# Optimization experiments

Measured on AMD Instinct MI355X. Metric: run time of the kernel, lower is better.

## Reference

```python
import jax, jax.numpy as jnp
import numpy as np

N_NODES = 100000
N_EDGES = 3200000
EMB_DIM = 128


def setup_inputs() -> dict:
    key = jax.random.key(0)
    k_emb, k_w1, k_w2, k_e = jax.random.split(key, 4)
    emb = jax.random.normal(k_emb, (N_NODES, EMB_DIM), dtype=jnp.float32)
    W1 = jax.random.normal(k_w1, (EMB_DIM, 64), dtype=jnp.float32) * (1.0 / np.sqrt(EMB_DIM))
    b1 = jnp.zeros((64,), dtype=jnp.float32)
    W2 = jax.random.normal(k_w2, (64, 32), dtype=jnp.float32) * (1.0 / np.sqrt(64))
    b2 = jnp.zeros((32,), dtype=jnp.float32)
    edge_index = jax.random.randint(k_e, (2, N_EDGES), 0, N_NODES, dtype=jnp.int64)
    return {"embedding": emb, "W1": W1, "b1": b1, "W2": W2, "b2": b2,
            "edge_index": edge_index}


def gcn_conv(x, W, b, src, dst, n):
    # PyG GCNConv defaults: add self-loops, symmetric normalization D^-1/2 (A+I) D^-1/2,
    # linear transform first, then gather-scale-scatter aggregation, then bias.
    xw = x @ W                                                  # [N, out]
    ones = jnp.ones(src.shape, dtype=xw.dtype)
    deg = jax.ops.segment_sum(ones, dst, num_segments=n) + 1.0  # in-degree + self-loop
    dis = jax.lax.rsqrt(deg)                                    # deg >= 1 always
    norm = dis[src] * dis[dst]                                  # [E]
    agg = jax.ops.segment_sum(xw[src] * norm[:, None], dst, num_segments=n)
    agg = agg + (dis * dis)[:, None] * xw                       # self-loop messages
    return agg + b


def reference(embedding, W1, b1, W2, b2, edge_index):
    n = embedding.shape[0]
    src, dst = edge_index[0], edge_index[1]
    # encode
    h = jax.nn.relu(gcn_conv(embedding, W1, b1, src, dst, n))
    z = gcn_conv(h, W2, b2, src, dst, n)                        # [N, 32]
    # decode: per-edge gather-dot-sigmoid
    logits = jnp.sum(z[src] * z[dst], axis=1)                   # [E]
    return jax.nn.sigmoid(logits)
```

## Files before the change

kernel.cpp:

```cpp
#include <hip/hip_runtime.h>
#include <hip/hip_bf16.h>
#include <math.h>

#define NN 100000
#define NE 3200000
#define NPAD 100096
#define NB 196
#define BN 512
#define EPB 8192
#define NBLK 391

__device__ __forceinline__ unsigned short bf16_of(float x) {
    __hip_bfloat16 h = __float2bfloat16(x);
    return *(unsigned short*)&h;
}
__device__ __forceinline__ unsigned pack2(float a, float b) {
    return (unsigned)bf16_of(a) | ((unsigned)bf16_of(b) << 16);
}
__device__ __forceinline__ float lo_f(unsigned u) { return __uint_as_float(u << 16); }
__device__ __forceinline__ float hi_f(unsigned u) { return __uint_as_float(u & 0xffff0000u); }
__device__ __forceinline__ void acc8(float* a, uint4 r) {
    a[0] += lo_f(r.x); a[1] += hi_f(r.x);
    a[2] += lo_f(r.y); a[3] += hi_f(r.y);
    a[4] += lo_f(r.z); a[5] += hi_f(r.z);
    a[6] += lo_f(r.w); a[7] += hi_f(r.w);
}

__global__ __launch_bounds__(256) void hist_kernel(const int* __restrict__ dst,
                                                   int* __restrict__ blkhist) {
    __shared__ int cnt[NB];
    int t = threadIdx.x;
    for (int i = t; i < NB; i += 256) cnt[i] = 0;
    __syncthreads();
    int e0 = blockIdx.x * EPB;
    int e1 = min(e0 + EPB, NE);
    for (int e = e0 + t; e < e1; e += 256) atomicAdd(&cnt[dst[e] >> 9], 1);
    __syncthreads();
    for (int i = t; i < NB; i += 256) blkhist[i * NBLK + blockIdx.x] = cnt[i];
}

__global__ __launch_bounds__(64) void scanA_kernel(int* __restrict__ blkhist,
                                                   int* __restrict__ totals) {
    int j = blockIdx.x, lane = threadIdx.x;
    int base = j * NBLK;
    int carry = 0;
    for (int c = 0; c < NBLK; c += 64) {
        int b = c + lane;
        int v = (b < NBLK) ? blkhist[base + b] : 0;
        int inc = v;
#pragma unroll
        for (int m = 1; m < 64; m <<= 1) {
            int u = __shfl_up(inc, m, 64);
            if (lane >= m) inc += u;
        }
        if (b < NBLK) blkhist[base + b] = carry + inc - v;
        carry += __shfl(inc, 63, 64);
    }
    if (lane == 0) totals[j] = carry;
}

__global__ __launch_bounds__(256) void scanB_kernel(const int* __restrict__ totals,
                                                    int* __restrict__ bucket_base) {
    __shared__ int sm[NB];
    int t = threadIdx.x;
    if (t < NB) sm[t] = totals[t];
    __syncthreads();
    if (t == 0) {
        int r = 0;
        for (int i = 0; i < NB; ++i) { bucket_base[i] = r; r += sm[i]; }
        bucket_base[NB] = r;
    }
}

__global__ __launch_bounds__(256) void scatter_kernel(const int* __restrict__ src,
                                                      const int* __restrict__ dst,
                                                      const int* __restrict__ blkhist,
                                                      const int* __restrict__ bucket_base,
                                                      int* __restrict__ staged) {
    __shared__ int cur[NB];
    int t = threadIdx.x;
    for (int i = t; i < NB; i += 256)
        cur[i] = bucket_base[i] + blkhist[i * NBLK + blockIdx.x];
    __syncthreads();
    int e0 = blockIdx.x * EPB;
    int e1 = min(e0 + EPB, NE);
    for (int e = e0 + t; e < e1; e += 256) {
        int s = src[e], d = dst[e];
        int p = atomicAdd(&cur[d >> 9], 1);
        staged[p] = (s << 9) | (d & (BN - 1));
    }
}

__global__ __launch_bounds__(256) void fine_kernel(const int* __restrict__ staged,
                                                   const int* __restrict__ bucket_base,
                                                   int* __restrict__ offset,
                                                   float* __restrict__ dis,
                                                   int* __restrict__ csr_src) {
    __shared__ int hist[BN];
    __shared__ int offs[BN];
    __shared__ int cur[BN];
    int t = threadIdx.x, j = blockIdx.x;
    int bb = bucket_base[j], be = bucket_base[j + 1];
    for (int i = t; i < BN; i += 256) hist[i] = 0;
    __syncthreads();
    for (int e = bb + t; e < be; e += 256) atomicAdd(&hist[staged[e] & (BN - 1)], 1);
    __syncthreads();
    if (t < 64) {
        int v[8]; int s = 0;
#pragma unroll
        for (int k = 0; k < 8; ++k) { v[k] = hist[t * 8 + k]; s += v[k]; }
        int inc = s;
#pragma unroll
        for (int m = 1; m < 64; m <<= 1) {
            int u = __shfl_up(inc, m, 64);
            if (t >= m) inc += u;
        }
        int run = inc - s;
#pragma unroll
        for (int k = 0; k < 8; ++k) { offs[t * 8 + k] = run; run += v[k]; }
    }
    __syncthreads();
    for (int l = t; l < BN; l += 256) {
        cur[l] = offs[l];
        int n = j * BN + l;
        if (n < NN) {
            offset[n] = bb + offs[l];
            dis[n] = rsqrtf((float)hist[l] + 1.0f);
        }
    }
    if (j == NB - 1 && t == 0) offset[NN] = NE;
    __syncthreads();
    for (int e = bb + t; e < be; e += 256) {
        int p = staged[e];
        int r = atomicAdd(&cur[p & (BN - 1)], 1);
        csr_src[bb + r] = p >> 9;
    }
}

__global__ __launch_bounds__(256) void mm1_kernel(const float* __restrict__ x,
                                                  const float* __restrict__ W,
                                                  const float* __restrict__ dis,
                                                  unsigned short* __restrict__ y) {
    __shared__ float Ws[128 * 64];
    __shared__ float xs[4][4][132];
    int t = threadIdx.x;
    for (int i = t; i < 128 * 64; i += 256) Ws[i] = W[i];
    int wave = t >> 6, lane = t & 63;
    int nsub = lane >> 4;
    int o4 = (lane & 15) * 4;
    int base = blockIdx.x * 16 + wave * 4;
#pragma unroll
    for (int r = 0; r < 4; ++r) {
        xs[wave][r][lane] = x[(size_t)(base + r) * 128 + lane];
        xs[wave][r][lane + 64] = x[(size_t)(base + r) * 128 + 64 + lane];
    }
    __syncthreads();
    float4 acc = {0.f, 0.f, 0.f, 0.f};
#pragma unroll 16
    for (int k = 0; k < 128; ++k) {
        float a = xs[wave][nsub][k];
        const float4 w = *(const float4*)&Ws[k * 64 + o4];
        acc.x = fmaf(a, w.x, acc.x);
        acc.y = fmaf(a, w.y, acc.y);
        acc.z = fmaf(a, w.z, acc.z);
        acc.w = fmaf(a, w.w, acc.w);
    }
    float sc = dis[base + nsub];
    ushort4 o;
    o.x = bf16_of(acc.x * sc); o.y = bf16_of(acc.y * sc);
    o.z = bf16_of(acc.z * sc); o.w = bf16_of(acc.w * sc);
    *(ushort4*)&y[(size_t)(base + nsub) * 64 + o4] = o;
}

__global__ __launch_bounds__(256) void mm2_kernel(const float* __restrict__ h,
                                                  const float* __restrict__ W,
                                                  const float* __restrict__ dis,
                                                  unsigned short* __restrict__ y) {
    __shared__ float Ws[64 * 32];
    __shared__ float hs[4][8][68];
    int t = threadIdx.x;
    for (int i = t; i < 64 * 32; i += 256) Ws[i] = W[i];
    int wave = t >> 6, lane = t & 63;
    int nsub = lane >> 3;
    int o4 = (lane & 7) * 4;
    int base = blockIdx.x * 32 + wave * 8;
#pragma unroll
    for (int r = 0; r < 8; ++r)
        hs[wave][r][lane] = h[(size_t)(base + r) * 64 + lane];
    __syncthreads();
    float4 acc = {0.f, 0.f, 0.f, 0.f};
#pragma unroll 16
    for (int k = 0; k < 64; ++k) {
        float a = hs[wave][nsub][k];
        const float4 w = *(const float4*)&Ws[k * 32 + o4];
        acc.x = fmaf(a, w.x, acc.x);
        acc.y = fmaf(a, w.y, acc.y);
        acc.z = fmaf(a, w.z, acc.z);
        acc.w = fmaf(a, w.w, acc.w);
    }
    float sc = dis[base + nsub];
    ushort4 o;
    o.x = bf16_of(acc.x * sc); o.y = bf16_of(acc.y * sc);
    o.z = bf16_of(acc.z * sc); o.w = bf16_of(acc.w * sc);
    *(ushort4*)&y[(size_t)(base + nsub) * 32 + o4] = o;
}

__global__ __launch_bounds__(256) void agg64_kernel(const uint4* __restrict__ ys4,
                                                    const float* __restrict__ dis,
                                                    const int* __restrict__ offset,
                                                    const int* __restrict__ csr_src,
                                                    const float* __restrict__ b,
                                                    float* __restrict__ h) {
    int tid = blockIdx.x * 256 + threadIdx.x;
    int nd = tid >> 3, c = tid & 7;
    if (nd >= NN) return;
    int start = offset[nd], end = offset[nd + 1];
    float acc[8] = {0, 0, 0, 0, 0, 0, 0, 0};
    acc8(acc, ys4[(size_t)nd * 8 + c]);
    int i = start;
    int n4 = start + ((end - start) & ~3);
    for (; i < n4; i += 4) {
        int s0 = csr_src[i], s1 = csr_src[i + 1], s2 = csr_src[i + 2], s3 = csr_src[i + 3];
        uint4 r0 = ys4[(size_t)s0 * 8 + c];
        uint4 r1 = ys4[(size_t)s1 * 8 + c];
        uint4 r2 = ys4[(size_t)s2 * 8 + c];
        uint4 r3 = ys4[(size_t)s3 * 8 + c];
        acc8(acc, r0); acc8(acc, r1); acc8(acc, r2); acc8(acc, r3);
    }
    for (; i < end; ++i) acc8(acc, ys4[(size_t)csr_src[i] * 8 + c]);
    float ds = dis[nd];
    const float4 bv0 = *(const float4*)&b[c * 8];
    const float4 bv1 = *(const float4*)&b[c * 8 + 4];
    float4 o0, o1;
    o0.x = fmaxf(fmaf(ds, acc[0], bv0.x), 0.f);
    o0.y = fmaxf(fmaf(ds, acc[1], bv0.y), 0.f);
    o0.z = fmaxf(fmaf(ds, acc[2], bv0.z), 0.f);
    o0.w = fmaxf(fmaf(ds, acc[3], bv0.w), 0.f);
    o1.x = fmaxf(fmaf(ds, acc[4], bv1.x), 0.f);
    o1.y = fmaxf(fmaf(ds, acc[5], bv1.y), 0.f);
    o1.z = fmaxf(fmaf(ds, acc[6], bv1.z), 0.f);
    o1.w = fmaxf(fmaf(ds, acc[7], bv1.w), 0.f);
    float* hp = &h[(size_t)nd * 64 + c * 8];
    *(float4*)hp = o0;
    *(float4*)(hp + 4) = o1;
}

__global__ __launch_bounds__(256) void agg32_kernel(const uint4* __restrict__ ys4,
                                                    const float* __restrict__ dis,
                                                    const int* __restrict__ offset,
                                                    const int* __restrict__ csr_src,
                                                    const float* __restrict__ b,
                                                    uint4* __restrict__ z4) {
    int tid = blockIdx.x * 256 + threadIdx.x;
    int nd = tid >> 2, c = tid & 3;
    if (nd >= NN) return;
    int start = offset[nd], end = offset[nd + 1];
    float acc[8] = {0, 0, 0, 0, 0, 0, 0, 0};
    acc8(acc, ys4[(size_t)nd * 4 + c]);
    int i = start;
    int n4 = start + ((end - start) & ~3);
    for (; i < n4; i += 4) {
        int s0 = csr_src[i], s1 = csr_src[i + 1], s2 = csr_src[i + 2], s3 = csr_src[i + 3];
        uint4 r0 = ys4[(size_t)s0 * 4 + c];
        uint4 r1 = ys4[(size_t)s1 * 4 + c];
        uint4 r2 = ys4[(size_t)s2 * 4 + c];
        uint4 r3 = ys4[(size_t)s3 * 4 + c];
        acc8(acc, r0); acc8(acc, r1); acc8(acc, r2); acc8(acc, r3);
    }
    for (; i < end; ++i) acc8(acc, ys4[(size_t)csr_src[i] * 4 + c]);
    float ds = dis[nd];
    const float4 bv0 = *(const float4*)&b[c * 8];
    const float4 bv1 = *(const float4*)&b[c * 8 + 4];
    uint4 o;
    o.x = pack2(fmaf(ds, acc[0], bv0.x), fmaf(ds, acc[1], bv0.y));
    o.y = pack2(fmaf(ds, acc[2], bv0.z), fmaf(ds, acc[3], bv0.w));
    o.z = pack2(fmaf(ds, acc[4], bv1.x), fmaf(ds, acc[5], bv1.y));
    o.w = pack2(fmaf(ds, acc[6], bv1.z), fmaf(ds, acc[7], bv1.w));
    z4[(size_t)nd * 4 + c] = o;
}

__global__ __launch_bounds__(256) void decode_kernel(const uint4* __restrict__ z4,
                                                     const int* __restrict__ src,
                                                     const int* __restrict__ dst,
                                                     float* __restrict__ out) {
    int tid = blockIdx.x * 256 + threadIdx.x;
    int e = tid >> 2, k = tid & 3;
    if (e >= NE) return;
    int s = src[e], d = dst[e];
    uint4 ra = z4[(size_t)s * 4 + k];
    uint4 rb = z4[(size_t)d * 4 + k];
    float acc;
    acc  = lo_f(ra.x) * lo_f(rb.x) + hi_f(ra.x) * hi_f(rb.x);
    acc += lo_f(ra.y) * lo_f(rb.y) + hi_f(ra.y) * hi_f(rb.y);
    acc += lo_f(ra.z) * lo_f(rb.z) + hi_f(ra.z) * hi_f(rb.z);
    acc += lo_f(ra.w) * lo_f(rb.w) + hi_f(ra.w) * hi_f(rb.w);
#pragma unroll
    for (int m = 2; m >= 1; m >>= 1) acc += __shfl_xor(acc, m, 4);
    if (k == 0) out[e] = 1.0f / (1.0f + expf(-acc));
}

extern "C" void kernel_launch(void* const* d_in, const int* in_sizes, int n_in,
                              void* d_out, int out_size, void* d_ws, size_t ws_size,
                              hipStream_t stream) {
    const float* emb = (const float*)d_in[0];
    const float* W1  = (const float*)d_in[1];
    const float* b1  = (const float*)d_in[2];
    const float* W2  = (const float*)d_in[3];
    const float* b2  = (const float*)d_in[4];
    const int*   ei  = (const int*)d_in[5];
    const int* src = ei;
    const int* dst = ei + NE;
    float* out = (float*)d_out;

    char* w = (char*)d_ws;
    int*   offset      = (int*)w;           w += (size_t)NPAD * 4;
    float* dis         = (float*)w;         w += (size_t)NPAD * 4;
    int*   bucket_base = (int*)w;           w += 1024;
    int*   totals      = (int*)w;           w += 1024;
    int*   blkhist     = (int*)w;           w += 307200;
    int*   csr_src     = (int*)w;           w += (size_t)NE * 4;
    int*   staged      = (int*)w;           w += (size_t)NE * 4;
    unsigned short* ysbuf = (unsigned short*)w; w += (size_t)NN * 64 * 2;
    float* h           = (float*)w;
    unsigned short* ys1 = ysbuf;
    unsigned short* ys2 = ysbuf;
    unsigned short* z   = ysbuf + (size_t)NN * 32;

    hist_kernel<<<NBLK, 256, 0, stream>>>(dst, blkhist);
    scanA_kernel<<<NB, 64, 0, stream>>>(blkhist, totals);
    scanB_kernel<<<1, 256, 0, stream>>>(totals, bucket_base);
    scatter_kernel<<<NBLK, 256, 0, stream>>>(src, dst, blkhist, bucket_base, staged);
    fine_kernel<<<NB, 256, 0, stream>>>(staged, bucket_base, offset, dis, csr_src);

    mm1_kernel<<<NN / 16, 256, 0, stream>>>(emb, W1, dis, ys1);
    agg64_kernel<<<(NN * 8) / 256, 256, 0, stream>>>((const uint4*)ys1, dis, offset, csr_src, b1, h);

    mm2_kernel<<<NN / 32, 256, 0, stream>>>(h, W2, dis, ys2);
    agg32_kernel<<<(NN * 4 + 255) / 256, 256, 0, stream>>>((const uint4*)ys2, dis, offset, csr_src, b2, (uint4*)z);

    decode_kernel<<<(NE * 4) / 256, 256, 0, stream>>>((const uint4*)z, src, dst, out);
}
```

Before: 401.0 us.

## Stage scatter in LDS, store hidden layer as bf16, widen matmul and gather unroll

```diff
diff --git a/kernel.cpp b/kernel.cpp
--- a/kernel.cpp
+++ b/kernel.cpp
@@ -77,17 +77,49 @@
                                                       const int* __restrict__ blkhist,
                                                       const int* __restrict__ bucket_base,
                                                       int* __restrict__ staged) {
-    __shared__ int cur[NB];
-    int t = threadIdx.x;
-    for (int i = t; i < NB; i += 256)
-        cur[i] = bucket_base[i] + blkhist[i * NBLK + blockIdx.x];
+    __shared__ int cnt[NB];
+    __shared__ int lbase[NB + 1];
+    __shared__ int gbase[NB];
+    __shared__ int sbuf[EPB];
+    int t = threadIdx.x;
+    for (int i = t; i < NB; i += 256) cnt[i] = 0;
     __syncthreads();
     int e0 = blockIdx.x * EPB;
     int e1 = min(e0 + EPB, NE);
+    int cn = e1 - e0;
+    for (int e = e0 + t; e < e1; e += 256) atomicAdd(&cnt[dst[e] >> 9], 1);
+    __syncthreads();
+    if (t < 64) {
+        int v[4]; int s = 0;
+#pragma unroll
+        for (int k = 0; k < 4; ++k) { int idx = t * 4 + k; v[k] = (idx < NB) ? cnt[idx] : 0; s += v[k]; }
+        int inc = s;
+#pragma unroll
+        for (int m = 1; m < 64; m <<= 1) {
+            int u = __shfl_up(inc, m, 64);
+            if (t >= m) inc += u;
+        }
+        int run = inc - s;
+#pragma unroll
+        for (int k = 0; k < 4; ++k) { int idx = t * 4 + k; if (idx < NB) lbase[idx] = run; run += v[k]; }
+        if (t == 63) lbase[NB] = inc;
+    }
+    __syncthreads();
+    for (int i = t; i < NB; i += 256) {
+        gbase[i] = bucket_base[i] + blkhist[i * NBLK + blockIdx.x];
+        cnt[i] = lbase[i];
+    }
+    __syncthreads();
     for (int e = e0 + t; e < e1; e += 256) {
         int s = src[e], d = dst[e];
-        int p = atomicAdd(&cur[d >> 9], 1);
-        staged[p] = (s << 9) | (d & (BN - 1));
+        int r = atomicAdd(&cnt[d >> 9], 1);
+        sbuf[r] = (s << 9) | (d & (BN - 1));
+    }
+    __syncthreads();
+    for (int i = t; i < cn; i += 256) {
+        int lo = 0, hi = NB - 1;
+        while (lo < hi) { int mid = (lo + hi + 1) >> 1; if (lbase[mid] <= i) lo = mid; else hi = mid - 1; }
+        staged[gbase[lo] + i - lbase[lo]] = sbuf[i];
     }
 }
 
@@ -142,37 +174,40 @@
                                                   const float* __restrict__ dis,
                                                   unsigned short* __restrict__ y) {
     __shared__ float Ws[128 * 64];
-    __shared__ float xs[4][4][132];
+    __shared__ float xs[4][8][132];
     int t = threadIdx.x;
     for (int i = t; i < 128 * 64; i += 256) Ws[i] = W[i];
     int wave = t >> 6, lane = t & 63;
-    int nsub = lane >> 4;
-    int o4 = (lane & 15) * 4;
-    int base = blockIdx.x * 16 + wave * 4;
-#pragma unroll
-    for (int r = 0; r < 4; ++r) {
+    int nsub = lane >> 3;
+    int o8 = (lane & 7) * 8;
+    int base = blockIdx.x * 32 + wave * 8;
+#pragma unroll
+    for (int r = 0; r < 8; ++r) {
         xs[wave][r][lane] = x[(size_t)(base + r) * 128 + lane];
         xs[wave][r][lane + 64] = x[(size_t)(base + r) * 128 + 64 + lane];
     }
     __syncthreads();
-    float4 acc = {0.f, 0.f, 0.f, 0.f};
+    float acc[8] = {0, 0, 0, 0, 0, 0, 0, 0};
 #pragma unroll 16
     for (int k = 0; k < 128; ++k) {
         float a = xs[wave][nsub][k];
-        const float4 w = *(const float4*)&Ws[k * 64 + o4];
-        acc.x = fmaf(a, w.x, acc.x);
-        acc.y = fmaf(a, w.y, acc.y);
-        acc.z = fmaf(a, w.z, acc.z);
-        acc.w = fmaf(a, w.w, acc.w);
+        const float4 w0 = *(const float4*)&Ws[k * 64 + o8];
+        const float4 w1 = *(const float4*)&Ws[k * 64 + o8 + 4];
+        acc[0] = fmaf(a, w0.x, acc[0]); acc[1] = fmaf(a, w0.y, acc[1]);
+        acc[2] = fmaf(a, w0.z, acc[2]); acc[3] = fmaf(a, w0.w, acc[3]);
+        acc[4] = fmaf(a, w1.x, acc[4]); acc[5] = fmaf(a, w1.y, acc[5]);
+        acc[6] = fmaf(a, w1.z, acc[6]); acc[7] = fmaf(a, w1.w, acc[7]);
     }
     float sc = dis[base + nsub];
-    ushort4 o;
-    o.x = bf16_of(acc.x * sc); o.y = bf16_of(acc.y * sc);
-    o.z = bf16_of(acc.z * sc); o.w = bf16_of(acc.w * sc);
-    *(ushort4*)&y[(size_t)(base + nsub) * 64 + o4] = o;
-}
-
-__global__ __launch_bounds__(256) void mm2_kernel(const float* __restrict__ h,
+    uint4 o;
+    o.x = pack2(acc[0] * sc, acc[1] * sc);
+    o.y = pack2(acc[2] * sc, acc[3] * sc);
+    o.z = pack2(acc[4] * sc, acc[5] * sc);
+    o.w = pack2(acc[6] * sc, acc[7] * sc);
+    *(uint4*)&y[(size_t)(base + nsub) * 64 + o8] = o;
+}
+
+__global__ __launch_bounds__(256) void mm2_kernel(const unsigned short* __restrict__ h,
                                                   const float* __restrict__ W,
                                                   const float* __restrict__ dis,
                                                   unsigned short* __restrict__ y) {
@@ -184,9 +219,14 @@
     int nsub = lane >> 3;
     int o4 = (lane & 7) * 4;
     int base = blockIdx.x * 32 + wave * 8;
-#pragma unroll
-    for (int r = 0; r < 8; ++r)
-        hs[wave][r][lane] = h[(size_t)(base + r) * 64 + lane];
+    const unsigned* h2 = (const unsigned*)h;
+#pragma unroll
+    for (int rr = 0; rr < 4; ++rr) {
+        int r = rr * 2 + (lane >> 5);
+        unsigned u = h2[(size_t)(base + r) * 32 + (lane & 31)];
+        hs[wave][r][(lane & 31) * 2] = lo_f(u);
+        hs[wave][r][(lane & 31) * 2 + 1] = hi_f(u);
+    }
     __syncthreads();
     float4 acc = {0.f, 0.f, 0.f, 0.f};
 #pragma unroll 16
@@ -210,7 +250,7 @@
                                                     const int* __restrict__ offset,
                                                     const int* __restrict__ csr_src,
                                                     const float* __restrict__ b,
-                                                    float* __restrict__ h) {
+                                                    uint4* __restrict__ h4) {
     int tid = blockIdx.x * 256 + threadIdx.x;
     int nd = tid >> 3, c = tid & 7;
     if (nd >= NN) return;
@@ -218,31 +258,31 @@
     float acc[8] = {0, 0, 0, 0, 0, 0, 0, 0};
     acc8(acc, ys4[(size_t)nd * 8 + c]);
     int i = start;
-    int n4 = start + ((end - start) & ~3);
-    for (; i < n4; i += 4) {
-        int s0 = csr_src[i], s1 = csr_src[i + 1], s2 = csr_src[i + 2], s3 = csr_src[i + 3];
+    int n8 = start + ((end - start) & ~7);
+    for (; i < n8; i += 8) {
+        int s0 = csr_src[i],     s1 = csr_src[i + 1], s2 = csr_src[i + 2], s3 = csr_src[i + 3];
+        int s4 = csr_src[i + 4], s5 = csr_src[i + 5], s6 = csr_src[i + 6], s7 = csr_src[i + 7];
         uint4 r0 = ys4[(size_t)s0 * 8 + c];
         uint4 r1 = ys4[(size_t)s1 * 8 + c];
         uint4 r2 = ys4[(size_t)s2 * 8 + c];
         uint4 r3 = ys4[(size_t)s3 * 8 + c];
+        uint4 r4 = ys4[(size_t)s4 * 8 + c];
+        uint4 r5 = ys4[(size_t)s5 * 8 + c];
+        uint4 r6 = ys4[(size_t)s6 * 8 + c];
+        uint4 r7 = ys4[(size_t)s7 * 8 + c];
         acc8(acc, r0); acc8(acc, r1); acc8(acc, r2); acc8(acc, r3);
+        acc8(acc, r4); acc8(acc, r5); acc8(acc, r6); acc8(acc, r7);
     }
     for (; i < end; ++i) acc8(acc, ys4[(size_t)csr_src[i] * 8 + c]);
     float ds = dis[nd];
     const float4 bv0 = *(const float4*)&b[c * 8];
     const float4 bv1 = *(const float4*)&b[c * 8 + 4];
-    float4 o0, o1;
-    o0.x = fmaxf(fmaf(ds, acc[0], bv0.x), 0.f);
-    o0.y = fmaxf(fmaf(ds, acc[1], bv0.y), 0.f);
-    o0.z = fmaxf(fmaf(ds, acc[2], bv0.z), 0.f);
-    o0.w = fmaxf(fmaf(ds, acc[3], bv0.w), 0.f);
-    o1.x = fmaxf(fmaf(ds, acc[4], bv1.x), 0.f);
-    o1.y = fmaxf(fmaf(ds, acc[5], bv1.y), 0.f);
-    o1.z = fmaxf(fmaf(ds, acc[6], bv1.z), 0.f);
-    o1.w = fmaxf(fmaf(ds, acc[7], bv1.w), 0.f);
-    float* hp = &h[(size_t)nd * 64 + c * 8];
-    *(float4*)hp = o0;
-    *(float4*)(hp + 4) = o1;
+    uint4 o;
+    o.x = pack2(fmaxf(fmaf(ds, acc[0], bv0.x), 0.f), fmaxf(fmaf(ds, acc[1], bv0.y), 0.f));
+    o.y = pack2(fmaxf(fmaf(ds, acc[2], bv0.z), 0.f), fmaxf(fmaf(ds, acc[3], bv0.w), 0.f));
+    o.z = pack2(fmaxf(fmaf(ds, acc[4], bv1.x), 0.f), fmaxf(fmaf(ds, acc[5], bv1.y), 0.f));
+    o.w = pack2(fmaxf(fmaf(ds, acc[6], bv1.z), 0.f), fmaxf(fmaf(ds, acc[7], bv1.w), 0.f));
+    h4[(size_t)nd * 8 + c] = o;
 }
 
 __global__ __launch_bounds__(256) void agg32_kernel(const uint4* __restrict__ ys4,
@@ -258,14 +298,20 @@
     float acc[8] = {0, 0, 0, 0, 0, 0, 0, 0};
     acc8(acc, ys4[(size_t)nd * 4 + c]);
     int i = start;
-    int n4 = start + ((end - start) & ~3);
-    for (; i < n4; i += 4) {
-        int s0 = csr_src[i], s1 = csr_src[i + 1], s2 = csr_src[i + 2], s3 = csr_src[i + 3];
+    int n8 = start + ((end - start) & ~7);
+    for (; i < n8; i += 8) {
+        int s0 = csr_src[i],     s1 = csr_src[i + 1], s2 = csr_src[i + 2], s3 = csr_src[i + 3];
+        int s4 = csr_src[i + 4], s5 = csr_src[i + 5], s6 = csr_src[i + 6], s7 = csr_src[i + 7];
         uint4 r0 = ys4[(size_t)s0 * 4 + c];
         uint4 r1 = ys4[(size_t)s1 * 4 + c];
         uint4 r2 = ys4[(size_t)s2 * 4 + c];
         uint4 r3 = ys4[(size_t)s3 * 4 + c];
+        uint4 r4 = ys4[(size_t)s4 * 4 + c];
+        uint4 r5 = ys4[(size_t)s5 * 4 + c];
+        uint4 r6 = ys4[(size_t)s6 * 4 + c];
+        uint4 r7 = ys4[(size_t)s7 * 4 + c];
         acc8(acc, r0); acc8(acc, r1); acc8(acc, r2); acc8(acc, r3);
+        acc8(acc, r4); acc8(acc, r5); acc8(acc, r6); acc8(acc, r7);
     }
     for (; i < end; ++i) acc8(acc, ys4[(size_t)csr_src[i] * 4 + c]);
     float ds = dis[nd];
@@ -321,7 +367,7 @@
     int*   csr_src     = (int*)w;           w += (size_t)NE * 4;
     int*   staged      = (int*)w;           w += (size_t)NE * 4;
     unsigned short* ysbuf = (unsigned short*)w; w += (size_t)NN * 64 * 2;
-    float* h           = (float*)w;
+    unsigned short* h  = (unsigned short*)w;
     unsigned short* ys1 = ysbuf;
     unsigned short* ys2 = ysbuf;
     unsigned short* z   = ysbuf + (size_t)NN * 32;
@@ -332,8 +378,8 @@
     scatter_kernel<<<NBLK, 256, 0, stream>>>(src, dst, blkhist, bucket_base, staged);
     fine_kernel<<<NB, 256, 0, stream>>>(staged, bucket_base, offset, dis, csr_src);
 
-    mm1_kernel<<<NN / 16, 256, 0, stream>>>(emb, W1, dis, ys1);
-    agg64_kernel<<<(NN * 8) / 256, 256, 0, stream>>>((const uint4*)ys1, dis, offset, csr_src, b1, h);
+    mm1_kernel<<<NN / 32, 256, 0, stream>>>(emb, W1, dis, ys1);
+    agg64_kernel<<<(NN * 8) / 256, 256, 0, stream>>>((const uint4*)ys1, dis, offset, csr_src, b1, (uint4*)h);
 
     mm2_kernel<<<NN / 32, 256, 0, stream>>>(h, W2, dis, ys2);
     agg32_kernel<<<(NN * 4 + 255) / 256, 256, 0, stream>>>((const uint4*)ys2, dis, offset, csr_src, b2, (uint4*)z);
```

Result: no change. 398.3 us (-0.7%).
